# Kernel optimization log

Hardware: AMD Instinct MI355X
Metric: run time of the kernel (lower is better)

Reference implementation:

```python
import jax, jax.numpy as jnp
import numpy as np

N_ATOMS = 50000   # nAtoms
KMAX = 32         # max neighbors per atom
EMB_ATOM = 256    # emb_size_atom
EMB_PAIR_IN = 64  # emb_size_pair_in
EMB_PAIR_OUT = 64 # emb_size_pair_out
EMB_RBF = 16      # emb_size_rbf
INV_SQRT = lambda n: 1.0 / np.sqrt(n).astype(np.float32)


def setup_inputs() -> dict:
    key = jax.random.key(0)
    k_h, k_rb, k_src, k_wd, k_wb, k_wu = jax.random.split(key, 6)
    h = jax.random.normal(k_h, (N_ATOMS, EMB_ATOM), dtype=jnp.float32)
    rad_basis = jax.random.normal(k_rb, (N_ATOMS, EMB_RBF, KMAX), dtype=jnp.float32)
    # each destination atom has exactly KMAX neighbors -> unique (dst, slot) pairs
    dst = jnp.repeat(jnp.arange(N_ATOMS, dtype=jnp.int64), KMAX)
    src = jax.random.randint(k_src, (N_ATOMS * KMAX,), 0, N_ATOMS, dtype=jnp.int64)
    edge_index = jnp.stack([src, dst])  # (2, nEdges)
    target_neighbor_idx = jnp.tile(jnp.arange(KMAX, dtype=jnp.int64), N_ATOMS)
    W_down = jax.random.normal(k_wd, (EMB_ATOM, EMB_PAIR_IN), dtype=jnp.float32) * INV_SQRT(EMB_ATOM)
    W_bilinear = jax.random.normal(k_wb, (EMB_RBF * EMB_PAIR_IN, EMB_PAIR_OUT), dtype=jnp.float32) * INV_SQRT(EMB_RBF * EMB_PAIR_IN)
    W_up = jax.random.normal(k_wu, (EMB_PAIR_OUT, EMB_ATOM), dtype=jnp.float32) * INV_SQRT(EMB_PAIR_OUT)
    return {"h": h, "rad_basis": rad_basis, "edge_index": edge_index,
            "target_neighbor_idx": target_neighbor_idx,
            "W_down": W_down, "W_bilinear": W_bilinear, "W_up": W_up}


def reference(h, rad_basis, edge_index, target_neighbor_idx, W_down, W_bilinear, W_up):
    num_atoms = h.shape[0]
    kmax = rad_basis.shape[-1]
    # down projection (no bias, no activation)
    x_b = h @ W_down                               # (nAtoms, emb_pair_in)
    x_ba = x_b[edge_index[0]]                      # (nEdges, emb_pair_in) gather from source atoms
    # scatter into dense padded tensor (nAtoms, Kmax, emb_pair_in)
    x2 = jnp.zeros((num_atoms, kmax, x_ba.shape[-1]), dtype=x_ba.dtype)
    x2 = x2.at[edge_index[1], target_neighbor_idx].set(x_ba)
    # per-atom batched matmul with radial basis: (nAtoms, emb_rbf, Kmax) @ (nAtoms, Kmax, emb_pair_in)
    x_ba2 = jnp.einsum('nrk,nkp->nrp', rad_basis, x2)
    # bilinear projection on flattened (emb_rbf * emb_pair_in); ScaleFactor default scale = 1.0 (identity)
    h_out = x_ba2.reshape(num_atoms, -1) @ W_bilinear  # (nAtoms, emb_pair_out)
    return h_out @ W_up                               # (nAtoms, emb_size_atom)
```

## Files before the change

kernel.cpp:

```cpp
#include <hip/hip_runtime.h>

#define N_ATOMS 50000
#define KMAX 32
#define EMB_ATOM 256
#define EP_IN 64
#define EP_OUT 64
#define EMB_RBF 16
#define NEDGES (N_ATOMS * KMAX)

typedef _Float16 half_t;
typedef __attribute__((ext_vector_type(2))) _Float16 half2_t;
typedef __attribute__((ext_vector_type(4))) _Float16 half4_t;
typedef __attribute__((ext_vector_type(8))) _Float16 half8_t;
typedef __attribute__((ext_vector_type(4))) float f32x4;

static_assert(N_ATOMS % 16 == 0, "fused kernel assumes 16 atoms per block");

#define GLOAD_LDS16(g, l)                                                     \
    __builtin_amdgcn_global_load_lds(                                         \
        (const __attribute__((address_space(1))) void*)(g),                   \
        (__attribute__((address_space(3))) void*)(l), 16, 0, 0)

#define XB_NB 782
#define SC_NB (NEDGES / 256)
#define WB_NB 256
#define WU_NB 64
#define PREP_NB (XB_NB + SC_NB + WB_NB + WU_NB + 1)

__global__ __launch_bounds__(256) void prep_all(const float* __restrict__ h,
                                                const float* __restrict__ Wd,
                                                const int*   __restrict__ ei,
                                                const int*   __restrict__ tni,
                                                const float* __restrict__ Wb,
                                                const float* __restrict__ Wu,
                                                half_t* __restrict__ xbh,
                                                int*    __restrict__ sidx,
                                                half_t* __restrict__ Wb2,
                                                half_t* __restrict__ Wu2,
                                                half_t* __restrict__ zrow) {
    __shared__ float As[16 * 68];
    __shared__ float Bs[16 * 64];
    const int bid = blockIdx.x;
    const int t = threadIdx.x;

    if (bid < XB_NB) {
        const int r0 = bid * 64;
        const int tr = t >> 4, tc = t & 15;
        float acc[4][4] = {};
        for (int k0 = 0; k0 < 256; k0 += 16) {
            {
                int m = t >> 2, kk0 = (t & 3) << 2;
                int row = r0 + m;
                float4 v = make_float4(0.f, 0.f, 0.f, 0.f);
                if (row < N_ATOMS)
                    v = *reinterpret_cast<const float4*>(&h[(size_t)row * 256 + k0 + kk0]);
                As[(kk0 + 0) * 68 + m] = v.x;
                As[(kk0 + 1) * 68 + m] = v.y;
                As[(kk0 + 2) * 68 + m] = v.z;
                As[(kk0 + 3) * 68 + m] = v.w;
            }
            {
                int kk = t >> 4, n0 = (t & 15) << 2;
                *reinterpret_cast<float4*>(&Bs[kk * 64 + n0]) =
                    *reinterpret_cast<const float4*>(&Wd[(k0 + kk) * 64 + n0]);
            }
            __syncthreads();
            #pragma unroll
            for (int kk = 0; kk < 16; ++kk) {
                float4 av = *reinterpret_cast<const float4*>(&As[kk * 68 + tr * 4]);
                float4 bv = *reinterpret_cast<const float4*>(&Bs[kk * 64 + tc * 4]);
                float aa[4] = {av.x, av.y, av.z, av.w};
                float bb[4] = {bv.x, bv.y, bv.z, bv.w};
                #pragma unroll
                for (int i = 0; i < 4; ++i)
                    #pragma unroll
                    for (int j = 0; j < 4; ++j) acc[i][j] += aa[i] * bb[j];
            }
            __syncthreads();
        }
        #pragma unroll
        for (int i = 0; i < 4; ++i) {
            int row = r0 + tr * 4 + i;
            if (row < N_ATOMS) {
                half4_t hv;
                #pragma unroll
                for (int j = 0; j < 4; ++j) hv[j] = (half_t)acc[i][j];
                *reinterpret_cast<half4_t*>(&xbh[(size_t)row * 64 + tc * 4]) = hv;
            }
        }
    } else if (bid < XB_NB + SC_NB) {
        int i = (bid - XB_NB) * 256 + t;
        int s = ei[i];
        int d = ei[NEDGES + i];
        int k = tni[i];
        sidx[d * KMAX + k] = s;
    } else if (bid < XB_NB + SC_NB + WB_NB) {
        int i = (bid - XB_NB - SC_NB) * 256 + t;
        int e = i & 7, lv = (i >> 3) & 63;
        int c = lv & 15, g = lv >> 4;
        int kh = (i >> 13) & 1, ot = i >> 14;
        int o = ot * 16 + c;
        int idx = kh * 512 + ((i >> 9) & 15) * 32 + g * 8 + e;
        int r = ((idx >> 6) & 3) * 4 + (idx & 3);
        int p = (idx >> 8) * 16 + ((idx >> 2) & 15);
        Wb2[i] = (half_t)Wb[(size_t)(r * 64 + p) * 64 + o];
    } else if (bid < XB_NB + SC_NB + WB_NB + WU_NB) {
        int i = (bid - XB_NB - SC_NB - WB_NB) * 256 + t;
        int e = i & 7, lv = (i >> 3) & 63;
        int c = lv & 15, g = lv >> 4;
        int kk = (i >> 9) & 1, nt = (i >> 10) & 1, w = i >> 11;
        int oc = w * 32 + nt * 16 + c;
        int o = kk * 32 + g * 8 + e;
        Wu2[i] = (half_t)Wu[(size_t)o * 256 + oc];
    } else {
        if (t < 128) zrow[t] = (half_t)0.f;
    }
}

__device__ __forceinline__ void consume_batch(const char* stb, int c, int g,
                                              half4_t radf, half4_t ident,
                                              f32x4 (&acc)[4]) {
    const f32x4 fzero = {0.f, 0.f, 0.f, 0.f};
    #pragma unroll
    for (int pc = 0; pc < 4; ++pc) {
        int slot = (pc * 2 + (g >> 1)) ^ (c & 7);
        half4_t gf = *reinterpret_cast<const half4_t*>(
            stb + c * 128 + slot * 16 + (g & 1) * 8);
        f32x4 tD = __builtin_amdgcn_mfma_f32_16x16x16f16(gf, ident, fzero, 0, 0, 0);
        half4_t b2;
        #pragma unroll
        for (int j = 0; j < 4; ++j) b2[j] = (half_t)tD[j];
        acc[pc] = __builtin_amdgcn_mfma_f32_16x16x16f16(radf, b2, acc[pc], 0, 0, 0);
    }
}

#define ISSUE(as, kc, bufb) do {                                              \
    _Pragma("unroll")                                                         \
    for (int h_ = 0; h_ < 2; ++h_) {                                          \
        int s_ = __shfl(sv, (as) * 32 + (kc) * 16 + h_ * 8 + (l >> 3), 64);   \
        const half_t* src_ = ((unsigned)s_ < (unsigned)N_ATOMS)               \
            ? (xbh + (size_t)s_ * 64) : zrow;                                 \
        src_ += (((l & 7) ^ (l >> 3)) << 3);          \
        GLOAD_LDS16(src_, (half_t*)(Rbase + (bufb)) + h_ * 512);              \
    }                                                                         \
} while (0)

#define WRITE_ATOM(a_, accv) do {                                             \
    _Pragma("unroll")                                                         \
    for (int pc = 0; pc < 4; ++pc) {                                          \
        half4_t hv;                                                           \
        _Pragma("unroll")                                                     \
        for (int j = 0; j < 4; ++j) hv[j] = (half_t)accv[pc][j];              \
        int byte_ = ((a_) * 2048 + pc * 512 + g * 128 + c * 8) ^              \
                    (((a_) & 7) << 4);                                        \
        *reinterpret_cast<half4_t*>(reinterpret_cast<char*>(xba2s) + byte_) = hv; \
    }                                                                         \
} while (0)

#define WAIT_VM(n) do {                                                       \
    asm volatile("s_waitcnt vmcnt(" #n ")" ::: "memory");                     \
    __builtin_amdgcn_sched_barrier(0);                                        \
} while (0)

#define WAIT_LGKM() do {                                                      \
    asm volatile("s_waitcnt lgkmcnt(0)" ::: "memory");                        \
    __builtin_amdgcn_sched_barrier(0);                                        \
} while (0)

__global__ __launch_bounds__(512, 6) void fused(const half_t* __restrict__ xbh,
                                                const float*  __restrict__ rad,
                                                const int*    __restrict__ sidxg,
                                                const half_t* __restrict__ Wb2,
                                                const half_t* __restrict__ Wu2,
                                                const half_t* __restrict__ zrow,
                                                float* __restrict__ out) {
    __shared__ __align__(16) half_t xba2s[16 * 1024];
    __shared__ __align__(16) float  preds[2 * 16 * 68];
    __shared__ __align__(16) half_t houts[16 * 64];

    const int t = threadIdx.x;
    const int w = t >> 6;
    const int l = t & 63;
    const int c = l & 15;
    const int g = l >> 4;
    const int a0 = blockIdx.x * 16;

    char* Rbase = reinterpret_cast<char*>(xba2s) + w * 4096;

    const f32x4 fzero = {0.f, 0.f, 0.f, 0.f};

    int sv = sidxg[(size_t)(a0 + w * 2) * KMAX + l];
    const float* radw = &rad[(size_t)(a0 + w * 2) * 512];
    f32x4 rv[4];
    #pragma unroll
    for (int q = 0; q < 4; ++q)
        rv[q] = *reinterpret_cast<const f32x4*>(radw + q * 256 + l * 4);

    ISSUE(0, 0, 0);
    ISSUE(0, 1, 2048);
    __builtin_amdgcn_sched_barrier(0);

    const int ot = w >> 1, kh = w & 1;
    const half_t* wbbase = &Wb2[(size_t)((ot * 2 + kh) * 16) * 512];
    half8_t bfr[4];
    #pragma unroll
    for (int j = 0; j < 4; ++j)
        bfr[j] = *reinterpret_cast<const half8_t*>(wbbase + j * 512 + l * 8);
    __builtin_amdgcn_sched_barrier(0);

    half4_t radF[2][2];
    #pragma unroll
    for (int as = 0; as < 2; ++as)
        #pragma unroll
        for (int kc = 0; kc < 2; ++kc) {
            int srcl = (c & 7) * 8 + kc * 4 + g;
            #pragma unroll
            for (int j = 0; j < 4; ++j) {
                float lo = __shfl(rv[as * 2 + 0][j], srcl, 64);
                float hi = __shfl(rv[as * 2 + 1][j], srcl, 64);
                radF[as][kc][j] = (half_t)((c & 8) ? hi : lo);
            }
        }

    half4_t ident;
    #pragma unroll
    for (int j = 0; j < 4; ++j) ident[j] = (half_t)((g * 4 + j == c) ? 1.0f : 0.0f);

    f32x4 acc0[4] = {fzero, fzero, fzero, fzero};
    f32x4 acc1[4] = {fzero, fzero, fzero, fzero};

    WAIT_VM(6);
    consume_batch(Rbase, c, g, radF[0][0], ident, acc0);
    WAIT_LGKM();
    ISSUE(1, 0, 0);
    WAIT_VM(6);
    consume_batch(Rbase + 2048, c, g, radF[0][1], ident, acc0);
    WAIT_LGKM();
    ISSUE(1, 1, 2048);
    WAIT_VM(2);
    consume_batch(Rbase, c, g, radF[1][0], ident, acc1);
    WRITE_ATOM(w * 2, acc0);
    WAIT_VM(0);
    consume_batch(Rbase + 2048, c, g, radF[1][1], ident, acc1);
    WRITE_ATOM(w * 2 + 1, acc1);

    __syncthreads();

    {
        f32x4 acc2[4] = {fzero, fzero, fzero, fzero};
        #pragma unroll
        for (int j = 0; j < 16; ++j) {
            int abyte = (c * 2048 + (kh * 512 + j * 32) * 2 + g * 16) ^ ((c & 7) << 4);
            half8_t af = *reinterpret_cast<const half8_t*>(
                reinterpret_cast<const char*>(xba2s) + abyte);
            half8_t bf = bfr[j & 3];
            if (j + 4 < 16)
                bfr[j & 3] = *reinterpret_cast<const half8_t*>(wbbase + (j + 4) * 512 + l * 8);
            acc2[j & 3] = __builtin_amdgcn_mfma_f32_16x16x32_f16(af, bf, acc2[j & 3], 0, 0, 0);
        }
        f32x4 accT = acc2[0] + acc2[1] + acc2[2] + acc2[3];
        #pragma unroll
        for (int i = 0; i < 4; ++i)
            preds[kh * 1088 + (g * 4 + i) * 68 + ot * 16 + c] = accT[i];
    }

    half8_t wuf[2][2];
    #pragma unroll
    for (int nt = 0; nt < 2; ++nt)
        #pragma unroll
        for (int kk = 0; kk < 2; ++kk)
            wuf[nt][kk] = *reinterpret_cast<const half8_t*>(
                &Wu2[(size_t)(((w * 2 + nt) * 2 + kk) * 64 + l) * 8]);

    __syncthreads();

    {
        int m = t >> 5, oj = (t & 31) << 1;
        float s0 = preds[m * 68 + oj]     + preds[1088 + m * 68 + oj];
        float s1 = preds[m * 68 + oj + 1] + preds[1088 + m * 68 + oj + 1];
        half2_t hv; hv[0] = (half_t)s0; hv[1] = (half_t)s1;
        int byte_ = (m * 128 + oj * 2) ^ ((m & 7) << 4);
        *reinterpret_cast<half2_t*>(reinterpret_cast<char*>(houts) + byte_) = hv;
    }
    __syncthreads();

    half8_t ha[2];
    #pragma unroll
    for (int kk = 0; kk < 2; ++kk) {
        int byte_ = (c * 128 + kk * 64 + g * 16) ^ ((c & 7) << 4);
        ha[kk] = *reinterpret_cast<const half8_t*>(
            reinterpret_cast<const char*>(houts) + byte_);
    }
    #pragma unroll
    for (int nt = 0; nt < 2; ++nt) {
        int oc0 = w * 32 + nt * 16;
        f32x4 acc3 = fzero;
        #pragma unroll
        for (int kk = 0; kk < 2; ++kk)
            acc3 = __builtin_amdgcn_mfma_f32_16x16x32_f16(ha[kk], wuf[nt][kk], acc3, 0, 0, 0);
        #pragma unroll
        for (int i = 0; i < 4; ++i)
            out[(size_t)(a0 + g * 4 + i) * 256 + oc0 + c] = acc3[i];
    }
}

extern "C" void kernel_launch(void* const* d_in, const int* in_sizes, int n_in,
                              void* d_out, int out_size, void* d_ws, size_t ws_size,
                              hipStream_t stream) {
    const float* h   = (const float*)d_in[0];
    const float* rad = (const float*)d_in[1];
    const int*   ei  = (const int*)d_in[2];
    const int*   tni = (const int*)d_in[3];
    const float* Wd  = (const float*)d_in[4];
    const float* Wb  = (const float*)d_in[5];
    const float* Wu  = (const float*)d_in[6];
    float* out = (float*)d_out;

    half_t* xbh  = (half_t*)d_ws;
    int*    sidx = (int*)((char*)d_ws + (size_t)N_ATOMS * EP_IN * sizeof(half_t));
    half_t* Wb2  = (half_t*)((char*)sidx + (size_t)NEDGES * sizeof(int));
    half_t* Wu2  = Wb2 + 64 * 1024;
    half_t* zrow = Wu2 + 16384;

    prep_all<<<PREP_NB, 256, 0, stream>>>(h, Wd, ei, tni, Wb, Wu,
                                          xbh, sidx, Wb2, Wu2, zrow);
    fused<<<N_ATOMS / 16, 512, 0, stream>>>(xbh, rad, sidx, Wb2, Wu2, zrow, out);
}
```

Measured before the change: 85.41 us.

## Process 32 atoms per block with full-K bilinear per wave

Doubles the atom tile per block from 16 to 32, so each wave gathers and contracts four atoms instead of two. The bilinear stage switches from a split-K layout with a float partial-sum reduction to each wave owning one 16-row tile and one output tile across the full 1024-wide K. That removes the preds buffer and one barrier, and the bilinear weights are loaded once per 32 atoms instead of per 16. In exchange it uses more LDS and registers (launch bounds drop to 4 waves per SIMD), halves the block count, and adds bounds clamps for a partial last tile.

```diff
diff --git a/kernel.cpp b/kernel.cpp
--- a/kernel.cpp
+++ b/kernel.cpp
@@ -14,7 +14,8 @@
 typedef __attribute__((ext_vector_type(8))) _Float16 half8_t;
 typedef __attribute__((ext_vector_type(4))) float f32x4;
 
-static_assert(N_ATOMS % 16 == 0, "fused kernel assumes 16 atoms per block");
+#define NATILE 32
+#define FUSED_NB ((N_ATOMS + NATILE - 1) / NATILE)
 
 #define GLOAD_LDS16(g, l)                                                     \
     __builtin_amdgcn_global_load_lds(                                         \
@@ -134,14 +135,14 @@
     }
 }
 
-#define ISSUE(as, kc, bufb) do {                                              \
+#define ISSUE2(a_, kc_, svv) do {                                             \
     _Pragma("unroll")                                                         \
     for (int h_ = 0; h_ < 2; ++h_) {                                          \
-        int s_ = __shfl(sv, (as) * 32 + (kc) * 16 + h_ * 8 + (l >> 3), 64);   \
+        int s_ = __shfl(svv, ((a_) & 1) * 32 + (kc_) * 16 + h_ * 8 + (l >> 3), 64); \
         const half_t* src_ = ((unsigned)s_ < (unsigned)N_ATOMS)               \
             ? (xbh + (size_t)s_ * 64) : zrow;                                 \
         src_ += (((l & 7) ^ (l >> 3)) << 3);          \
-        GLOAD_LDS16(src_, (half_t*)(Rbase + (bufb)) + h_ * 512);              \
+        GLOAD_LDS16(src_, (half_t*)(Rb + (a_) * 2048) + h_ * 512);            \
     }                                                                         \
 } while (0)
 
@@ -167,50 +168,56 @@
     __builtin_amdgcn_sched_barrier(0);                                        \
 } while (0)
 
-__global__ __launch_bounds__(512, 6) void fused(const half_t* __restrict__ xbh,
+#define SBAR() __builtin_amdgcn_sched_barrier(0)
+
+__global__ __launch_bounds__(512, 4) void fused(const half_t* __restrict__ xbh,
                                                 const float*  __restrict__ rad,
                                                 const int*    __restrict__ sidxg,
                                                 const half_t* __restrict__ Wb2,
                                                 const half_t* __restrict__ Wu2,
                                                 const half_t* __restrict__ zrow,
                                                 float* __restrict__ out) {
-    __shared__ __align__(16) half_t xba2s[16 * 1024];
-    __shared__ __align__(16) float  preds[2 * 16 * 68];
-    __shared__ __align__(16) half_t houts[16 * 64];
+    __shared__ __align__(16) half_t xba2s[32 * 1024];
+    __shared__ __align__(16) half_t houts[32 * 64];
 
     const int t = threadIdx.x;
     const int w = t >> 6;
     const int l = t & 63;
     const int c = l & 15;
     const int g = l >> 4;
-    const int a0 = blockIdx.x * 16;
-
-    char* Rbase = reinterpret_cast<char*>(xba2s) + w * 4096;
+    const int a0 = blockIdx.x * NATILE;
+
+    char* Rb = reinterpret_cast<char*>(xba2s) + w * 8192;
 
     const f32x4 fzero = {0.f, 0.f, 0.f, 0.f};
 
-    int sv = sidxg[(size_t)(a0 + w * 2) * KMAX + l];
-    const float* radw = &rad[(size_t)(a0 + w * 2) * 512];
-    f32x4 rv[4];
-    #pragma unroll
-    for (int q = 0; q < 4; ++q)
-        rv[q] = *reinterpret_cast<const f32x4*>(radw + q * 256 + l * 4);
-
-    ISSUE(0, 0, 0);
-    ISSUE(0, 1, 2048);
-    __builtin_amdgcn_sched_barrier(0);
-
-    const int ot = w >> 1, kh = w & 1;
-    const half_t* wbbase = &Wb2[(size_t)((ot * 2 + kh) * 16) * 512];
-    half8_t bfr[4];
+    int ga_s0 = a0 + w * 4 + (l >> 5);     if (ga_s0 > N_ATOMS - 1) ga_s0 = N_ATOMS - 1;
+    int ga_s1 = a0 + w * 4 + 2 + (l >> 5); if (ga_s1 > N_ATOMS - 1) ga_s1 = N_ATOMS - 1;
+    int sv0 = sidxg[(size_t)ga_s0 * KMAX + (l & 31)];
+    int sv1 = sidxg[(size_t)ga_s1 * KMAX + (l & 31)];
+    f32x4 rv[8];
+    #pragma unroll
+    for (int q = 0; q < 8; ++q) {
+        int ga = a0 + w * 4 + (q >> 1); if (ga > N_ATOMS - 1) ga = N_ATOMS - 1;
+        rv[q] = *reinterpret_cast<const f32x4*>(rad + (size_t)ga * 512 + (q & 1) * 256 + l * 4);
+    }
+    SBAR();
+    ISSUE2(0, 0, sv0);
+    ISSUE2(1, 0, sv0);
+    ISSUE2(2, 0, sv1);
+    ISSUE2(3, 0, sv1);
+    SBAR();
+    const int mt = w >> 2, ot = w & 3;
+    const half_t* wbbase = &Wb2[(size_t)ot * 16384];
+    half8_t bfr[8];
     #pragma unroll
     for (int j = 0; j < 4; ++j)
         bfr[j] = *reinterpret_cast<const half8_t*>(wbbase + j * 512 + l * 8);
-    __builtin_amdgcn_sched_barrier(0);
-
-    half4_t radF[2][2];
-    #pragma unroll
-    for (int as = 0; as < 2; ++as)
+    SBAR();
+
+    half4_t radF[4][2];
+    #pragma unroll
+    for (int as = 0; as < 4; ++as)
         #pragma unroll
         for (int kc = 0; kc < 2; ++kc) {
             int srcl = (c & 7) * 8 + kc * 4 + g;
@@ -226,42 +233,53 @@
     #pragma unroll
     for (int j = 0; j < 4; ++j) ident[j] = (half_t)((g * 4 + j == c) ? 1.0f : 0.0f);
 
-    f32x4 acc0[4] = {fzero, fzero, fzero, fzero};
-    f32x4 acc1[4] = {fzero, fzero, fzero, fzero};
-
-    WAIT_VM(6);
-    consume_batch(Rbase, c, g, radF[0][0], ident, acc0);
+    f32x4 accA[4] = {fzero, fzero, fzero, fzero};
+    f32x4 accB[4] = {fzero, fzero, fzero, fzero};
+    f32x4 accC[4] = {fzero, fzero, fzero, fzero};
+    f32x4 accD[4] = {fzero, fzero, fzero, fzero};
+
+    WAIT_VM(10);  consume_batch(Rb,        c, g, radF[0][0], ident, accA);
+    WAIT_LGKM();  ISSUE2(0, 1, sv0);
+    WAIT_VM(10);  consume_batch(Rb + 2048, c, g, radF[1][0], ident, accB);
+    WAIT_LGKM();  ISSUE2(1, 1, sv0);
+    WAIT_VM(10);  consume_batch(Rb + 4096, c, g, radF[2][0], ident, accC);
+    WAIT_LGKM();  ISSUE2(2, 1, sv1);
+    WAIT_VM(10);  consume_batch(Rb + 6144, c, g, radF[3][0], ident, accD);
+    WAIT_LGKM();  ISSUE2(3, 1, sv1);
+    WAIT_VM(6);   consume_batch(Rb,        c, g, radF[0][1], ident, accA);
+    WAIT_VM(4);   consume_batch(Rb + 2048, c, g, radF[1][1], ident, accB);
+    WAIT_VM(2);   consume_batch(Rb + 4096, c, g, radF[2][1], ident, accC);
+    WAIT_VM(0);   consume_batch(Rb + 6144, c, g, radF[3][1], ident, accD);
     WAIT_LGKM();
-    ISSUE(1, 0, 0);
-    WAIT_VM(6);
-    consume_batch(Rbase + 2048, c, g, radF[0][1], ident, acc0);
-    WAIT_LGKM();
-    ISSUE(1, 1, 2048);
-    WAIT_VM(2);
-    consume_batch(Rbase, c, g, radF[1][0], ident, acc1);
-    WRITE_ATOM(w * 2, acc0);
-    WAIT_VM(0);
-    consume_batch(Rbase + 2048, c, g, radF[1][1], ident, acc1);
-    WRITE_ATOM(w * 2 + 1, acc1);
+    WRITE_ATOM(w * 4 + 0, accA);
+    WRITE_ATOM(w * 4 + 1, accB);
+    WRITE_ATOM(w * 4 + 2, accC);
+    WRITE_ATOM(w * 4 + 3, accD);
+
+    #pragma unroll
+    for (int j = 4; j < 8; ++j)
+        bfr[j] = *reinterpret_cast<const half8_t*>(wbbase + j * 512 + l * 8);
 
     __syncthreads();
 
     {
         f32x4 acc2[4] = {fzero, fzero, fzero, fzero};
         #pragma unroll
-        for (int j = 0; j < 16; ++j) {
-            int abyte = (c * 2048 + (kh * 512 + j * 32) * 2 + g * 16) ^ ((c & 7) << 4);
+        for (int j = 0; j < 32; ++j) {
+            int abyte = ((mt * 16 + c) * 2048 + j * 64 + g * 16) ^ ((c & 7) << 4);
             half8_t af = *reinterpret_cast<const half8_t*>(
                 reinterpret_cast<const char*>(xba2s) + abyte);
-            half8_t bf = bfr[j & 3];
-            if (j + 4 < 16)
-                bfr[j & 3] = *reinterpret_cast<const half8_t*>(wbbase + (j + 4) * 512 + l * 8);
-            acc2[j & 3] = __builtin_amdgcn_mfma_f32_16x16x32_f16(af, bf, acc2[j & 3], 0, 0, 0);
+            acc2[j & 3] = __builtin_amdgcn_mfma_f32_16x16x32_f16(af, bfr[j & 7], acc2[j & 3], 0, 0, 0);
+            if (j < 24)
+                bfr[j & 7] = *reinterpret_cast<const half8_t*>(wbbase + (j + 8) * 512 + l * 8);
         }
         f32x4 accT = acc2[0] + acc2[1] + acc2[2] + acc2[3];
         #pragma unroll
-        for (int i = 0; i < 4; ++i)
-            preds[kh * 1088 + (g * 4 + i) * 68 + ot * 16 + c] = accT[i];
+        for (int i = 0; i < 4; ++i) {
+            int m = mt * 16 + g * 4 + i;
+            int byte_ = (m * 128 + (ot * 16 + c) * 2) ^ ((m & 7) << 4);
+            *reinterpret_cast<half_t*>(reinterpret_cast<char*>(houts) + byte_) = (half_t)accT[i];
+        }
     }
 
     half8_t wuf[2][2];
@@ -274,33 +292,27 @@
 
     __syncthreads();
 
-    {
-        int m = t >> 5, oj = (t & 31) << 1;
-        float s0 = preds[m * 68 + oj]     + preds[1088 + m * 68 + oj];
-        float s1 = preds[m * 68 + oj + 1] + preds[1088 + m * 68 + oj + 1];
-        half2_t hv; hv[0] = (half_t)s0; hv[1] = (half_t)s1;
-        int byte_ = (m * 128 + oj * 2) ^ ((m & 7) << 4);
-        *reinterpret_cast<half2_t*>(reinterpret_cast<char*>(houts) + byte_) = hv;
-    }
-    __syncthreads();
-
-    half8_t ha[2];
-    #pragma unroll
-    for (int kk = 0; kk < 2; ++kk) {
-        int byte_ = (c * 128 + kk * 64 + g * 16) ^ ((c & 7) << 4);
-        ha[kk] = *reinterpret_cast<const half8_t*>(
-            reinterpret_cast<const char*>(houts) + byte_);
-    }
-    #pragma unroll
-    for (int nt = 0; nt < 2; ++nt) {
-        int oc0 = w * 32 + nt * 16;
-        f32x4 acc3 = fzero;
-        #pragma unroll
-        for (int kk = 0; kk < 2; ++kk)
-            acc3 = __builtin_amdgcn_mfma_f32_16x16x32_f16(ha[kk], wuf[nt][kk], acc3, 0, 0, 0);
-        #pragma unroll
-        for (int i = 0; i < 4; ++i)
-            out[(size_t)(a0 + g * 4 + i) * 256 + oc0 + c] = acc3[i];
+    #pragma unroll
+    for (int mt2 = 0; mt2 < 2; ++mt2) {
+        half8_t ha[2];
+        #pragma unroll
+        for (int kk = 0; kk < 2; ++kk) {
+            int byte_ = ((mt2 * 16 + c) * 128 + kk * 64 + g * 16) ^ ((c & 7) << 4);
+            ha[kk] = *reinterpret_cast<const half8_t*>(
+                reinterpret_cast<const char*>(houts) + byte_);
+        }
+        #pragma unroll
+        for (int nt = 0; nt < 2; ++nt) {
+            f32x4 acc3 = fzero;
+            acc3 = __builtin_amdgcn_mfma_f32_16x16x32_f16(ha[0], wuf[nt][0], acc3, 0, 0, 0);
+            acc3 = __builtin_amdgcn_mfma_f32_16x16x32_f16(ha[1], wuf[nt][1], acc3, 0, 0, 0);
+            #pragma unroll
+            for (int i = 0; i < 4; ++i) {
+                int row = a0 + mt2 * 16 + g * 4 + i;
+                if (row < N_ATOMS)
+                    out[(size_t)row * 256 + w * 32 + nt * 16 + c] = acc3[i];
+            }
+        }
     }
 }
 
@@ -324,5 +336,5 @@
 
     prep_all<<<PREP_NB, 256, 0, stream>>>(h, Wd, ei, tni, Wb, Wu,
                                           xbh, sidx, Wb2, Wu2, zrow);
-    fused<<<N_ATOMS / 16, 512, 0, stream>>>(xbh, rad, sidx, Wb2, Wu2, zrow, out);
+    fused<<<FUSED_NB, 512, 0, stream>>>(xbh, rad, sidx, Wb2, Wu2, zrow, out);
 }
```

Result: slower. 93.83 us (+9.9%).

## Make fused kernel persistent with double-buffered LDS prefetch of next tile

Applied to the files above, without the earlier changes.

Replaces the one-block-per-16-atom-tile launch with a persistent grid of 512 blocks that loop over tiles. The gather and radial-basis loads for the next tile are issued into a second LDS buffer while the bilinear and up-projection stages of the current tile run. This is meant to hide gather latency and remove per-block prologue costs such as the Wu fragment loads. In exchange it doubles LDS use and lowers the occupancy hint to 4, so fewer waves are available to hide latency.

```diff
diff --git a/kernel.cpp b/kernel.cpp
--- a/kernel.cpp
+++ b/kernel.cpp
@@ -14,7 +14,8 @@
 typedef __attribute__((ext_vector_type(8))) _Float16 half8_t;
 typedef __attribute__((ext_vector_type(4))) float f32x4;
 
-static_assert(N_ATOMS % 16 == 0, "fused kernel assumes 16 atoms per block");
+#define NT 3125
+#define GRIDN 512
 
 #define GLOAD_LDS16(g, l)                                                     \
     __builtin_amdgcn_global_load_lds(                                         \
@@ -134,18 +135,18 @@
     }
 }
 
-#define ISSUE(as, kc, bufb) do {                                              \
+#define ISSUEX(svv, bp, as_, kc_, bofs) do {                                  \
     _Pragma("unroll")                                                         \
     for (int h_ = 0; h_ < 2; ++h_) {                                          \
-        int s_ = __shfl(sv, (as) * 32 + (kc) * 16 + h_ * 8 + (l >> 3), 64);   \
+        int s_ = __shfl(svv, (as_) * 32 + (kc_) * 16 + h_ * 8 + (l >> 3), 64);\
         const half_t* src_ = ((unsigned)s_ < (unsigned)N_ATOMS)               \
             ? (xbh + (size_t)s_ * 64) : zrow;                                 \
         src_ += (((l & 7) ^ (l >> 3)) << 3);          \
-        GLOAD_LDS16(src_, (half_t*)(Rbase + (bufb)) + h_ * 512);              \
+        GLOAD_LDS16(src_, (half_t*)((bp) + (bofs)) + h_ * 512);               \
     }                                                                         \
 } while (0)
 
-#define WRITE_ATOM(a_, accv) do {                                             \
+#define WRITE_ATOMX(bp, a_, accv) do {                                        \
     _Pragma("unroll")                                                         \
     for (int pc = 0; pc < 4; ++pc) {                                          \
         half4_t hv;                                                           \
@@ -153,7 +154,7 @@
         for (int j = 0; j < 4; ++j) hv[j] = (half_t)accv[pc][j];              \
         int byte_ = ((a_) * 2048 + pc * 512 + g * 128 + c * 8) ^              \
                     (((a_) & 7) << 4);                                        \
-        *reinterpret_cast<half4_t*>(reinterpret_cast<char*>(xba2s) + byte_) = hv; \
+        *reinterpret_cast<half4_t*>((bp) + byte_) = hv;                       \
     }                                                                         \
 } while (0)
 
@@ -167,14 +168,16 @@
     __builtin_amdgcn_sched_barrier(0);                                        \
 } while (0)
 
-__global__ __launch_bounds__(512, 6) void fused(const half_t* __restrict__ xbh,
+#define SBAR() __builtin_amdgcn_sched_barrier(0)
+
+__global__ __launch_bounds__(512, 4) void fused(const half_t* __restrict__ xbh,
                                                 const float*  __restrict__ rad,
                                                 const int*    __restrict__ sidxg,
                                                 const half_t* __restrict__ Wb2,
                                                 const half_t* __restrict__ Wu2,
                                                 const half_t* __restrict__ zrow,
                                                 float* __restrict__ out) {
-    __shared__ __align__(16) half_t xba2s[16 * 1024];
+    __shared__ __align__(16) half_t xba2s[2][16 * 1024];
     __shared__ __align__(16) float  preds[2 * 16 * 68];
     __shared__ __align__(16) half_t houts[16 * 64];
 
@@ -183,124 +186,148 @@
     const int l = t & 63;
     const int c = l & 15;
     const int g = l >> 4;
-    const int a0 = blockIdx.x * 16;
-
-    char* Rbase = reinterpret_cast<char*>(xba2s) + w * 4096;
+    const int ot = w >> 1, kh = w & 1;
 
     const f32x4 fzero = {0.f, 0.f, 0.f, 0.f};
 
-    int sv = sidxg[(size_t)(a0 + w * 2) * KMAX + l];
-    const float* radw = &rad[(size_t)(a0 + w * 2) * 512];
+    half4_t ident;
+    #pragma unroll
+    for (int j = 0; j < 4; ++j) ident[j] = (half_t)((g * 4 + j == c) ? 1.0f : 0.0f);
+
+    half8_t wuf[2][2];
+    #pragma unroll
+    for (int nt = 0; nt < 2; ++nt)
+        #pragma unroll
+        for (int kk = 0; kk < 2; ++kk)
+            wuf[nt][kk] = *reinterpret_cast<const half8_t*>(
+                &Wu2[(size_t)(((w * 2 + nt) * 2 + kk) * 64 + l) * 8]);
+
+    const half_t* wbbase = &Wb2[(size_t)((ot * 2 + kh) * 16) * 512];
+
+    int tile = blockIdx.x;
+    int p = 0;
+
+    int sv = sidxg[(size_t)(tile * 16 + w * 2) * KMAX + l];
     f32x4 rv[4];
     #pragma unroll
     for (int q = 0; q < 4; ++q)
-        rv[q] = *reinterpret_cast<const f32x4*>(radw + q * 256 + l * 4);
-
-    ISSUE(0, 0, 0);
-    ISSUE(0, 1, 2048);
-    __builtin_amdgcn_sched_barrier(0);
-
-    const int ot = w >> 1, kh = w & 1;
-    const half_t* wbbase = &Wb2[(size_t)((ot * 2 + kh) * 16) * 512];
-    half8_t bfr[4];
-    #pragma unroll
-    for (int j = 0; j < 4; ++j)
-        bfr[j] = *reinterpret_cast<const half8_t*>(wbbase + j * 512 + l * 8);
-    __builtin_amdgcn_sched_barrier(0);
-
-    half4_t radF[2][2];
-    #pragma unroll
-    for (int as = 0; as < 2; ++as)
-        #pragma unroll
-        for (int kc = 0; kc < 2; ++kc) {
-            int srcl = (c & 7) * 8 + kc * 4 + g;
-            #pragma unroll
-            for (int j = 0; j < 4; ++j) {
-                float lo = __shfl(rv[as * 2 + 0][j], srcl, 64);
-                float hi = __shfl(rv[as * 2 + 1][j], srcl, 64);
-                radF[as][kc][j] = (half_t)((c & 8) ? hi : lo);
-            }
-        }
-
-    half4_t ident;
-    #pragma unroll
-    for (int j = 0; j < 4; ++j) ident[j] = (half_t)((g * 4 + j == c) ? 1.0f : 0.0f);
-
-    f32x4 acc0[4] = {fzero, fzero, fzero, fzero};
-    f32x4 acc1[4] = {fzero, fzero, fzero, fzero};
-
-    WAIT_VM(6);
-    consume_batch(Rbase, c, g, radF[0][0], ident, acc0);
-    WAIT_LGKM();
-    ISSUE(1, 0, 0);
-    WAIT_VM(6);
-    consume_batch(Rbase + 2048, c, g, radF[0][1], ident, acc0);
-    WAIT_LGKM();
-    ISSUE(1, 1, 2048);
-    WAIT_VM(2);
-    consume_batch(Rbase, c, g, radF[1][0], ident, acc1);
-    WRITE_ATOM(w * 2, acc0);
-    WAIT_VM(0);
-    consume_batch(Rbase + 2048, c, g, radF[1][1], ident, acc1);
-    WRITE_ATOM(w * 2 + 1, acc1);
-
-    __syncthreads();
-
+        rv[q] = *reinterpret_cast<const f32x4*>(
+            rad + (size_t)(tile * 16 + w * 2) * 512 + q * 256 + l * 4);
     {
-        f32x4 acc2[4] = {fzero, fzero, fzero, fzero};
-        #pragma unroll
-        for (int j = 0; j < 16; ++j) {
-            int abyte = (c * 2048 + (kh * 512 + j * 32) * 2 + g * 16) ^ ((c & 7) << 4);
-            half8_t af = *reinterpret_cast<const half8_t*>(
-                reinterpret_cast<const char*>(xba2s) + abyte);
-            half8_t bf = bfr[j & 3];
-            if (j + 4 < 16)
-                bfr[j & 3] = *reinterpret_cast<const half8_t*>(wbbase + (j + 4) * 512 + l * 8);
-            acc2[j & 3] = __builtin_amdgcn_mfma_f32_16x16x32_f16(af, bf, acc2[j & 3], 0, 0, 0);
-        }
-        f32x4 accT = acc2[0] + acc2[1] + acc2[2] + acc2[3];
-        #pragma unroll
-        for (int i = 0; i < 4; ++i)
-            preds[kh * 1088 + (g * 4 + i) * 68 + ot * 16 + c] = accT[i];
+        char* Rb0 = reinterpret_cast<char*>(&xba2s[0][0]) + w * 4096;
+        ISSUEX(sv, Rb0, 0, 0, 0);
+        ISSUEX(sv, Rb0, 0, 1, 2048);
     }
-
-    half8_t wuf[2][2];
-    #pragma unroll
-    for (int nt = 0; nt < 2; ++nt)
-        #pragma unroll
-        for (int kk = 0; kk < 2; ++kk)
-            wuf[nt][kk] = *reinterpret_cast<const half8_t*>(
-                &Wu2[(size_t)(((w * 2 + nt) * 2 + kk) * 64 + l) * 8]);
-
-    __syncthreads();
-
-    {
-        int m = t >> 5, oj = (t & 31) << 1;
-        float s0 = preds[m * 68 + oj]     + preds[1088 + m * 68 + oj];
-        float s1 = preds[m * 68 + oj + 1] + preds[1088 + m * 68 + oj + 1];
-        half2_t hv; hv[0] = (half_t)s0; hv[1] = (half_t)s1;
-        int byte_ = (m * 128 + oj * 2) ^ ((m & 7) << 4);
-        *reinterpret_cast<half2_t*>(reinterpret_cast<char*>(houts) + byte_) = hv;
-    }
-    __syncthreads();
-
-    half8_t ha[2];
-    #pragma unroll
-    for (int kk = 0; kk < 2; ++kk) {
-        int byte_ = (c * 128 + kk * 64 + g * 16) ^ ((c & 7) << 4);
-        ha[kk] = *reinterpret_cast<const half8_t*>(
-            reinterpret_cast<const char*>(houts) + byte_);
-    }
-    #pragma unroll
-    for (int nt = 0; nt < 2; ++nt) {
-        int oc0 = w * 32 + nt * 16;
-        f32x4 acc3 = fzero;
-        #pragma unroll
-        for (int kk = 0; kk < 2; ++kk)
-            acc3 = __builtin_amdgcn_mfma_f32_16x16x32_f16(ha[kk], wuf[nt][kk], acc3, 0, 0, 0);
-        #pragma unroll
-        for (int i = 0; i < 4; ++i)
-            out[(size_t)(a0 + g * 4 + i) * 256 + oc0 + c] = acc3[i];
+    SBAR();
+
+    while (tile < NT) {
+        char* Xp = reinterpret_cast<char*>(&xba2s[p][0]);
+        char* Rb = Xp + w * 4096;
+        const int a0 = tile * 16;
+
+        half4_t radF[2][2];
+        #pragma unroll
+        for (int as = 0; as < 2; ++as)
+            #pragma unroll
+            for (int kc = 0; kc < 2; ++kc) {
+                int srcl = (c & 7) * 8 + kc * 4 + g;
+                #pragma unroll
+                for (int j = 0; j < 4; ++j) {
+                    float lo = __shfl(rv[as * 2 + 0][j], srcl, 64);
+                    float hi = __shfl(rv[as * 2 + 1][j], srcl, 64);
+                    radF[as][kc][j] = (half_t)((c & 8) ? hi : lo);
+                }
+            }
+
+        int tn = tile + GRIDN;
+        int tnc = (tn < NT) ? tn : tile;
+        int sv_next = sidxg[(size_t)(tnc * 16 + w * 2) * KMAX + l];
+        SBAR();
+
+        f32x4 acc0[4] = {fzero, fzero, fzero, fzero};
+        f32x4 acc1[4] = {fzero, fzero, fzero, fzero};
+
+        WAIT_VM(1);
+        consume_batch(Rb, c, g, radF[0][0], ident, acc0);
+        WAIT_LGKM(); ISSUEX(sv, Rb, 1, 0, 0);
+        consume_batch(Rb + 2048, c, g, radF[0][1], ident, acc0);
+        WAIT_LGKM(); ISSUEX(sv, Rb, 1, 1, 2048);
+        WAIT_VM(2);
+        consume_batch(Rb, c, g, radF[1][0], ident, acc1);
+        WRITE_ATOMX(Xp, w * 2, acc0);
+        WAIT_VM(0);
+        consume_batch(Rb + 2048, c, g, radF[1][1], ident, acc1);
+        WRITE_ATOMX(Xp, w * 2 + 1, acc1);
+
+        if (tn < NT) {
+            #pragma unroll
+            for (int q = 0; q < 4; ++q)
+                rv[q] = *reinterpret_cast<const f32x4*>(
+                    rad + (size_t)(tn * 16 + w * 2) * 512 + q * 256 + l * 4);
+            char* Rn = reinterpret_cast<char*>(&xba2s[p ^ 1][0]) + w * 4096;
+            ISSUEX(sv_next, Rn, 0, 0, 0);
+            ISSUEX(sv_next, Rn, 0, 1, 2048);
+        }
+        sv = sv_next;
+        SBAR();
+
+        half8_t bfr[8];
+        #pragma unroll
+        for (int j = 0; j < 8; ++j)
+            bfr[j] = *reinterpret_cast<const half8_t*>(wbbase + j * 512 + l * 8);
+        SBAR();
+
+        __syncthreads();
+
+        {
+            f32x4 acc2[4] = {fzero, fzero, fzero, fzero};
+            #pragma unroll
+            for (int j = 0; j < 16; ++j) {
+                int abyte = (c * 2048 + (kh * 512 + j * 32) * 2 + g * 16) ^ ((c & 7) << 4);
+                half8_t af = *reinterpret_cast<const half8_t*>(Xp + abyte);
+                acc2[j & 3] = __builtin_amdgcn_mfma_f32_16x16x32_f16(af, bfr[j & 7], acc2[j & 3], 0, 0, 0);
+                if (j < 8)
+                    bfr[j & 7] = *reinterpret_cast<const half8_t*>(wbbase + (j + 8) * 512 + l * 8);
+            }
+            f32x4 accT = acc2[0] + acc2[1] + acc2[2] + acc2[3];
+            #pragma unroll
+            for (int i = 0; i < 4; ++i)
+                preds[kh * 1088 + (g * 4 + i) * 68 + ot * 16 + c] = accT[i];
+        }
+        __syncthreads();
+
+        {
+            int m = t >> 5, oj = (t & 31) << 1;
+            float s0 = preds[m * 68 + oj]     + preds[1088 + m * 68 + oj];
+            float s1 = preds[m * 68 + oj + 1] + preds[1088 + m * 68 + oj + 1];
+            half2_t hv; hv[0] = (half_t)s0; hv[1] = (half_t)s1;
+            int byte_ = (m * 128 + oj * 2) ^ ((m & 7) << 4);
+            *reinterpret_cast<half2_t*>(reinterpret_cast<char*>(houts) + byte_) = hv;
+        }
+        __syncthreads();
+
+        {
+            half8_t ha[2];
+            #pragma unroll
+            for (int kk = 0; kk < 2; ++kk) {
+                int byte_ = (c * 128 + kk * 64 + g * 16) ^ ((c & 7) << 4);
+                ha[kk] = *reinterpret_cast<const half8_t*>(
+                    reinterpret_cast<const char*>(houts) + byte_);
+            }
+            #pragma unroll
+            for (int nt = 0; nt < 2; ++nt) {
+                int oc0 = w * 32 + nt * 16;
+                f32x4 acc3 = fzero;
+                acc3 = __builtin_amdgcn_mfma_f32_16x16x32_f16(ha[0], wuf[nt][0], acc3, 0, 0, 0);
+                acc3 = __builtin_amdgcn_mfma_f32_16x16x32_f16(ha[1], wuf[nt][1], acc3, 0, 0, 0);
+                #pragma unroll
+                for (int i = 0; i < 4; ++i)
+                    out[(size_t)(a0 + g * 4 + i) * 256 + oc0 + c] = acc3[i];
+            }
+        }
+
+        tile += GRIDN;
+        p ^= 1;
     }
 }
 
@@ -324,5 +351,5 @@
 
     prep_all<<<PREP_NB, 256, 0, stream>>>(h, Wd, ei, tni, Wb, Wu,
                                           xbh, sidx, Wb2, Wu2, zrow);
-    fused<<<N_ATOMS / 16, 512, 0, stream>>>(xbh, rad, sidx, Wb2, Wu2, zrow, out);
+    fused<<<GRIDN, 512, 0, stream>>>(xbh, rad, sidx, Wb2, Wu2, zrow, out);
 }
```

Measured after the change: 143.5 us. 68.1% more time.
